# Performance work log

Measured on AMD Instinct MI355X. Metric: run time of the kernel, lower is better.

The kernel has to match this reference:

```python
import jax, jax.numpy as jnp
import numpy as np

N_FFT = 1024
HOP = 256
B = 8
T = 2048  # n_frames
FREQ = N_FFT // 2 + 1


def setup_inputs() -> dict:
    key = jax.random.key(0)
    k1, k2 = jax.random.split(key)
    real_stft = jax.random.normal(k1, (B, 1, T, FREQ), dtype=jnp.float32)
    imag_stft = jax.random.normal(k2, (B, 1, T, FREQ), dtype=jnp.float32)
    # Build DFT synthesis matrices (same as torch module __init__, scaled=False)
    n = np.arange(N_FFT)
    hann = (0.5 - 0.5 * np.cos(2.0 * np.pi * n / N_FFT))  # fftbins=True hann
    ang = 2.0 * np.pi * np.outer(n, n) / N_FFT            # [k, n]
    W_real = (np.cos(ang) * hann[None, :] / N_FFT).astype(np.float32)
    W_imag = (np.sin(ang) * hann[None, :] / N_FFT).astype(np.float32)
    ola_window = (hann ** 2).astype(np.float32)
    return {
        "real_stft": real_stft,
        "imag_stft": imag_stft,
        "W_real": jnp.asarray(W_real),
        "W_imag": jnp.asarray(W_imag),
        "ola_window": jnp.asarray(ola_window),
    }


def reference(real_stft, imag_stft, W_real, W_imag, ola_window):
    n_fft = W_real.shape[0]
    b, _, n_frames, _ = real_stft.shape
    # (B, T, F) -> (B, F, T)
    fr = jnp.swapaxes(real_stft[:, 0], 1, 2)
    fi = jnp.swapaxes(imag_stft[:, 0], 1, 2)
    # Hermitian extension to full spectrum (B, n_fft, T)
    full_r = jnp.concatenate([fr, jnp.flip(fr[:, 1:-1, :], axis=1)], axis=1)
    full_i = jnp.concatenate([fi, -jnp.flip(fi[:, 1:-1, :], axis=1)], axis=1)
    # 1x1-conv DFT projection: out[b,t,n] = sum_k W[k,n] * x[b,k,t]
    frames = (jnp.einsum('kn,bkt->btn', W_real, full_r)
              - jnp.einsum('kn,bkt->btn', W_imag, full_i))  # (B, T, n_fft)
    out_len = (n_frames - 1) * HOP + n_fft
    # Overlap-add fold via scatter-add
    idx = (jnp.arange(n_frames)[:, None] * HOP + jnp.arange(n_fft)[None, :]).reshape(-1)
    y = jnp.zeros((b, out_len), frames.dtype).at[:, idx].add(frames.reshape(b, -1))
    # Window-sum fold + normalization
    wsum = jnp.zeros((out_len,), frames.dtype).at[idx].add(jnp.tile(ola_window, n_frames))
    wsum = jnp.clip(wsum, 1e-11, None)
    y = y / wsum[None, :]
    half = n_fft // 2
    return y[:, half:out_len - half]
```

## Files before the change

kernel.cpp:

```cpp
#include <hip/hip_runtime.h>


#define BATCH    8
#define NFRAMES  2048
#define FREQ     513
#define OUTCOLS  524032
#define FRAMES_B ((size_t)16384 * 1024 * 2)
#define TW_OFF   FRAMES_B
#define HANN_OFF (FRAMES_B + 16384)
#define WS_NEED  (FRAMES_B + 16384 + 4096)

typedef __attribute__((ext_vector_type(2))) float f32x2;
typedef __attribute__((ext_vector_type(4))) float f32x4;
typedef __attribute__((ext_vector_type(2))) unsigned uint2v;

__device__ __forceinline__ unsigned short f2bf(float x) {
    unsigned u = __float_as_uint(x);
    return (unsigned short)((u + 0x7fffu + ((u >> 16) & 1u)) >> 16);
}

__device__ __forceinline__ f32x2 cmul(f32x2 u, f32x4 w4) {
    return (f32x2){u[0], u[0]} * (f32x2){w4[0], w4[1]}
         + (f32x2){u[1], u[1]} * (f32x2){w4[2], w4[3]};
}

__global__ __launch_bounds__(256) void table_prep(const float* __restrict__ ola,
                                                  float* __restrict__ tw4,
                                                  float* __restrict__ hann) {
    int k = blockIdx.x * 256 + threadIdx.x;
    float s, c;
    sincosf(6.283185307179586f * (float)k * (1.0f / 1024.0f), &s, &c);
    ((f32x4*)tw4)[k] = (f32x4){c, s, -s, c};
    hann[k] = sqrtf(ola[k]) * (1.0f / 1024.0f);
}

__global__ __launch_bounds__(256) void ifft_frames6(
    const float* __restrict__ re, const float* __restrict__ im,
    const float* __restrict__ twg, const float* __restrict__ hann,
    unsigned short* __restrict__ frames) {
    __shared__ f32x2 X[1088], Y[1088];

    const int r0  = blockIdx.x * 2;
    const int tid = threadIdx.x;
    const f32x4* tw4 = (const f32x4*)twg;
    const int rpd = tid + (tid >> 4);

    const float* fre0 = re + (size_t)r0 * FREQ;
    const float* fim0 = im + (size_t)r0 * FREQ;
    const float* fre1 = fre0 + FREQ;
    const float* fim1 = fim0 + FREQ;

    {
        f32x2 a, b, c, d;
        {
            float A1 = fre0[tid], B1 = fim0[tid];
            float A2 = fre1[tid], B2 = fim1[tid];
            if (tid == 0) { B1 = 0.0f; B2 = 0.0f; }
            a = (f32x2){A1 - B2, B1 + A2};
        }
        {
            float A1 = fre0[tid + 256], B1 = fim0[tid + 256];
            float A2 = fre1[tid + 256], B2 = fim1[tid + 256];
            b = (f32x2){A1 - B2, B1 + A2};
        }
        {
            int m = 512 - tid;
            float A1 = fre0[m], B1 = fim0[m];
            float A2 = fre1[m], B2 = fim1[m];
            if (tid == 0) { B1 = 0.0f; B2 = 0.0f; }
            c = (f32x2){A1 + B2, A2 - B1};
        }
        {
            int m = 256 - tid;
            float A1 = fre0[m], B1 = fim0[m];
            float A2 = fre1[m], B2 = fim1[m];
            d = (f32x2){A1 + B2, A2 - B1};
        }
        f32x2 apc = a + c, amc = a - c, bpd = b + d, bmd = b - d;
        f32x2 jb = (f32x2){-bmd[1], bmd[0]};
        f32x4 w1 = tw4[tid], w2 = tw4[2 * tid], w3 = tw4[3 * tid];
        const int wb = 4 * tid + (tid >> 2);
        Y[wb]     = apc + bpd;
        Y[wb + 1] = cmul(amc + jb, w1);
        Y[wb + 2] = cmul(apc - bpd, w2);
        Y[wb + 3] = cmul(amc - jb, w3);
    }
    __syncthreads();

#define STAGE(S, P, Q, WBASE, O, RB, WB)                                      \
    {                                                                         \
        const int p  = (P);                                                   \
        const int t1 = p * (S);                                               \
        f32x4 w1 = tw4[t1], w2 = tw4[2 * t1], w3 = tw4[3 * t1];               \
        f32x2 a = RB[rpd],       b = RB[rpd + 272];                           \
        f32x2 c = RB[rpd + 544], d = RB[rpd + 816];                           \
        f32x2 apc = a + c, amc = a - c, bpd = b + d, bmd = b - d;             \
        f32x2 jb = (f32x2){-bmd[1], bmd[0]};                                  \
        const int wb = (WBASE);                                               \
        WB[wb]           = apc + bpd;                                         \
        WB[wb + (O)]     = cmul(amc + jb, w1);                                \
        WB[wb + 2 * (O)] = cmul(apc - bpd, w2);                               \
        WB[wb + 3 * (O)] = cmul(amc - jb, w3);                                \
        __syncthreads();                                                      \
    }

    STAGE(4,  tid >> 2, tid & 3,  17 * (tid >> 2) + (tid & 3),  4,  Y, X)
    STAGE(16, tid >> 4, tid & 15, 68 * (tid >> 4) + (tid & 15), 17, X, Y)
    STAGE(64, tid >> 6, tid & 63,
          272 * (tid >> 6) + (tid & 63) + ((tid & 63) >> 4),    68, Y, X)
#undef STAGE

    {
        f32x2 a = X[rpd],       b = X[rpd + 272];
        f32x2 c = X[rpd + 544], d = X[rpd + 816];
        f32x2 apc = a + c, amc = a - c, bpd = b + d, bmd = b - d;
        f32x2 jb = (f32x2){-bmd[1], bmd[0]};
        f32x2 y0 = apc + bpd;
        f32x2 y1 = amc + jb;
        f32x2 y2 = apc - bpd;
        f32x2 y3 = amc - jb;

        unsigned short* fR = frames + (size_t)r0 * 1024;
        unsigned short* fI = fR + 1024;
        float s0 = hann[tid];
        float s1 = hann[tid + 256];
        float s2 = hann[tid + 512];
        float s3 = hann[tid + 768];
        fR[tid]       = f2bf(y0[0] * s0);  fI[tid]       = f2bf(y0[1] * s0);
        fR[tid + 256] = f2bf(y1[0] * s1);  fI[tid + 256] = f2bf(y1[1] * s1);
        fR[tid + 512] = f2bf(y2[0] * s2);  fI[tid + 512] = f2bf(y2[1] * s2);
        fR[tid + 768] = f2bf(y3[0] * s3);  fI[tid + 768] = f2bf(y3[1] * s3);
    }
}

__global__ __launch_bounds__(256) void ola_fold4(
    const unsigned short* __restrict__ frames, const float* __restrict__ ola,
    float* __restrict__ out) {
    const int col0 = (blockIdx.x * 256 + threadIdx.x) * 4;
    if (col0 >= OUTCOLS) return;
    const int b  = blockIdx.y;
    const int s  = col0 + 512;
    const int g  = s >> 8;
    const int ls = s & 255;

    float a0 = 0.f, a1 = 0.f, a2 = 0.f, a3 = 0.f;
    float w0 = 0.f, w1 = 0.f, w2 = 0.f, w3 = 0.f;
#pragma unroll
    for (int j = 0; j < 4; ++j) {
        const int t = g - j;
        if (t >= 0 && t < NFRAMES) {
            uint2v u = *(const uint2v*)(frames + (((size_t)(b * NFRAMES + t)) << 10) + ls + 256 * j);
            a0 += __uint_as_float(u[0] << 16);
            a1 += __uint_as_float(u[0] & 0xffff0000u);
            a2 += __uint_as_float(u[1] << 16);
            a3 += __uint_as_float(u[1] & 0xffff0000u);
            f32x4 o = *(const f32x4*)(ola + ls + 256 * j);
            w0 += o[0]; w1 += o[1]; w2 += o[2]; w3 += o[3];
        }
    }
    f32x4 r = (f32x4){a0 / fmaxf(w0, 1e-11f), a1 / fmaxf(w1, 1e-11f),
                      a2 / fmaxf(w2, 1e-11f), a3 / fmaxf(w3, 1e-11f)};
    *(f32x4*)(out + (size_t)b * OUTCOLS + col0) = r;
}

__global__ __launch_bounds__(256) void istft_naive(
    const float* __restrict__ re, const float* __restrict__ im,
    const float* __restrict__ Wr, const float* __restrict__ Wi,
    const float* __restrict__ ola, float* __restrict__ out) {
    const int g = blockIdx.x + 2, b = blockIdx.y, ls = threadIdx.x;
    __shared__ float s_fr[4][FREQ];
    __shared__ float s_fi[4][FREQ];
#pragma unroll
    for (int jj = 0; jj < 4; ++jj) {
        const int t = g - jj;
        const bool valid = (t >= 0 && t < NFRAMES);
        const size_t base = ((size_t)b * NFRAMES + (valid ? t : 0)) * FREQ;
        for (int k = ls; k < FREQ; k += 256) {
            const float f = (k == 0 || k == FREQ - 1) ? 1.0f : 2.0f;
            s_fr[jj][k] = valid ? re[base + k] * f : 0.0f;
            s_fi[jj][k] = valid ? im[base + k] * f : 0.0f;
        }
    }
    __syncthreads();
    const float* wr = Wr + ls;
    const float* wi = Wi + ls;
    float acc = 0.0f;
    for (int k = 0; k < FREQ; ++k) {
        const float* wrk = wr + (size_t)k * 1024;
        const float* wik = wi + (size_t)k * 1024;
#pragma unroll
        for (int jj = 0; jj < 4; ++jj) {
            acc = fmaf(wrk[jj * 256], s_fr[jj][k], acc);
            acc = fmaf(-wik[jj * 256], s_fi[jj][k], acc);
        }
    }
    float wsv = 0.0f;
#pragma unroll
    for (int jj = 0; jj < 4; ++jj) {
        const int t = g - jj;
        if (t >= 0 && t < NFRAMES) wsv += ola[ls + jj * 256];
    }
    wsv = fmaxf(wsv, 1e-11f);
    out[(size_t)b * OUTCOLS + (g * 256 + ls - 512)] = acc / wsv;
}

extern "C" void kernel_launch(void* const* d_in, const int* in_sizes, int n_in,
                              void* d_out, int out_size, void* d_ws, size_t ws_size,
                              hipStream_t stream) {
    const float* re  = (const float*)d_in[0];
    const float* im  = (const float*)d_in[1];
    const float* Wr  = (const float*)d_in[2];
    const float* Wi  = (const float*)d_in[3];
    const float* ola = (const float*)d_in[4];
    float* out = (float*)d_out;

    if (ws_size >= WS_NEED) {
        unsigned short* frames = (unsigned short*)d_ws;
        float* tw   = (float*)((char*)d_ws + TW_OFF);
        float* hann = (float*)((char*)d_ws + HANN_OFF);
        hipLaunchKernelGGL(table_prep, dim3(4), dim3(256), 0, stream, ola, tw, hann);
        hipLaunchKernelGGL(ifft_frames6, dim3(8192), dim3(256), 0, stream,
                           re, im, tw, hann, frames);
        hipLaunchKernelGGL(ola_fold4, dim3(512, BATCH), dim3(256), 0, stream,
                           frames, ola, out);
    } else {
        dim3 grid(2047, BATCH);
        hipLaunchKernelGGL(istft_naive, grid, dim3(256), 0, stream,
                           re, im, Wr, Wi, ola, out);
    }
}
```

Baseline: 42.11 us.

## Run each 1024-point iFFT pair in a single wavefront with register radix-16 stages

The inverse FFT kernel now uses one 64-lane wavefront per frame pair instead of a 256-thread block. Each lane keeps 16 points in registers and fuses two radix-4 stages per pass, so there are only two LDS exchanges instead of four. This cuts shared-memory round trips and halves the LDS footprint. In exchange it raises register pressure, gives fewer threads per block, and loads the strided inputs less coalesced.

```diff
diff --git a/kernel.cpp b/kernel.cpp
--- a/kernel.cpp
+++ b/kernel.cpp
@@ -34,103 +34,119 @@
     hann[k] = sqrtf(ola[k]) * (1.0f / 1024.0f);
 }
 
-__global__ __launch_bounds__(256) void ifft_frames6(
+__global__ __launch_bounds__(64, 4) void ifft_wave(
     const float* __restrict__ re, const float* __restrict__ im,
     const float* __restrict__ twg, const float* __restrict__ hann,
     unsigned short* __restrict__ frames) {
-    __shared__ f32x2 X[1088], Y[1088];
-
-    const int r0  = blockIdx.x * 2;
-    const int tid = threadIdx.x;
+    __shared__ f32x2 L[1088];
+
+    const int l  = threadIdx.x;
+    const int r0 = blockIdx.x * 2;
     const f32x4* tw4 = (const f32x4*)twg;
-    const int rpd = tid + (tid >> 4);
 
     const float* fre0 = re + (size_t)r0 * FREQ;
     const float* fim0 = im + (size_t)r0 * FREQ;
     const float* fre1 = fre0 + FREQ;
     const float* fim1 = fim0 + FREQ;
 
+#define BFLY(IA, IB, IC, ID, T1, O0, O1, O2, O3)                              \
+    {                                                                         \
+        f32x2 apc = (IA) + (IC), amc = (IA) - (IC);                           \
+        f32x2 bpd = (IB) + (ID), bmd = (IB) - (ID);                           \
+        f32x2 jb  = (f32x2){-bmd[1], bmd[0]};                    \
+        O0 = apc + bpd;                                                       \
+        O1 = cmul(amc + jb, w1##T1);                                          \
+        O2 = cmul(apc - bpd, w2##T1);                                         \
+        O3 = cmul(amc - jb, w3##T1);                                          \
+    }
+
+    f32x2 s1[4][4];
+#pragma unroll
+    for (int j = 0; j < 4; ++j) {
+        f32x2 in[4];
+#pragma unroll
+        for (int k = 0; k < 4; ++k) {
+            int n  = l + 64 * j + 256 * k;
+            int mm = (n <= 512) ? n : (1024 - n);
+            float A1 = fre0[mm], B1 = fim0[mm];
+            float A2 = fre1[mm], B2 = fim1[mm];
+            if (n == 0 || n == 512) { B1 = 0.0f; B2 = 0.0f; }
+            in[k] = (n <= 512) ? (f32x2){A1 - B2, B1 + A2}
+                               : (f32x2){A1 + B2, A2 - B1};
+        }
+        const int t1 = l + 64 * j;
+        f32x4 w1A = tw4[t1], w2A = tw4[2 * t1], w3A = tw4[3 * t1];
+        BFLY(in[0], in[1], in[2], in[3], A, s1[j][0], s1[j][1], s1[j][2], s1[j][3]);
+    }
+
     {
-        f32x2 a, b, c, d;
-        {
-            float A1 = fre0[tid], B1 = fim0[tid];
-            float A2 = fre1[tid], B2 = fim1[tid];
-            if (tid == 0) { B1 = 0.0f; B2 = 0.0f; }
-            a = (f32x2){A1 - B2, B1 + A2};
-        }
-        {
-            float A1 = fre0[tid + 256], B1 = fim0[tid + 256];
-            float A2 = fre1[tid + 256], B2 = fim1[tid + 256];
-            b = (f32x2){A1 - B2, B1 + A2};
-        }
-        {
-            int m = 512 - tid;
-            float A1 = fre0[m], B1 = fim0[m];
-            float A2 = fre1[m], B2 = fim1[m];
-            if (tid == 0) { B1 = 0.0f; B2 = 0.0f; }
-            c = (f32x2){A1 + B2, A2 - B1};
-        }
-        {
-            int m = 256 - tid;
-            float A1 = fre0[m], B1 = fim0[m];
-            float A2 = fre1[m], B2 = fim1[m];
-            d = (f32x2){A1 + B2, A2 - B1};
-        }
+        const int t1 = 4 * l;
+        f32x4 w1B = tw4[t1], w2B = tw4[2 * t1], w3B = tw4[3 * t1];
+#pragma unroll
+        for (int r = 0; r < 4; ++r) {
+            f32x2 o0, o1, o2, o3;
+            BFLY(s1[0][r], s1[1][r], s1[2][r], s1[3][r], B, o0, o1, o2, o3);
+            int n0 = 16 * l + r;
+            L[n0      + (n0 >> 4)]        = o0;
+            L[n0 + 4  + ((n0 + 4) >> 4)]  = o1;
+            L[n0 + 8  + ((n0 + 8) >> 4)]  = o2;
+            L[n0 + 12 + ((n0 + 12) >> 4)] = o3;
+        }
+    }
+    __syncthreads();
+
+    f32x2 s3[4][4];
+#pragma unroll
+    for (int j = 0; j < 4; ++j) {
+        f32x2 in[4];
+#pragma unroll
+        for (int k = 0; k < 4; ++k) {
+            int n = l + 64 * j + 256 * k;
+            in[k] = L[n + (n >> 4)];
+        }
+        const int t1 = ((l + 64 * j) >> 4) << 4;
+        f32x4 w1C = tw4[t1], w2C = tw4[2 * t1], w3C = tw4[3 * t1];
+        BFLY(in[0], in[1], in[2], in[3], C, s3[j][0], s3[j][1], s3[j][2], s3[j][3]);
+    }
+    __syncthreads();
+
+    {
+        const int t1 = (l >> 4) << 6;
+        f32x4 w1D = tw4[t1], w2D = tw4[2 * t1], w3D = tw4[3 * t1];
+#pragma unroll
+        for (int r = 0; r < 4; ++r) {
+            f32x2 o0, o1, o2, o3;
+            BFLY(s3[0][r], s3[1][r], s3[2][r], s3[3][r], D, o0, o1, o2, o3);
+            int n0 = 256 * (l >> 4) + 16 * r + (l & 15);
+            int n1 = n0 + 64, n2 = n0 + 128, n3 = n0 + 192;
+            L[n0 + (n0 >> 4)] = o0;
+            L[n1 + (n1 >> 4)] = o1;
+            L[n2 + (n2 >> 4)] = o2;
+            L[n3 + (n3 >> 4)] = o3;
+        }
+    }
+    __syncthreads();
+
+    unsigned short* fR = frames + (size_t)r0 * 1024;
+    unsigned short* fI = fR + 1024;
+#pragma unroll
+    for (int h = 0; h < 4; ++h) {
+        int n0 = l + 64 * h;
+        int n1 = n0 + 256, n2 = n0 + 512, n3 = n0 + 768;
+        f32x2 a = L[n0 + (n0 >> 4)];
+        f32x2 b = L[n1 + (n1 >> 4)];
+        f32x2 c = L[n2 + (n2 >> 4)];
+        f32x2 d = L[n3 + (n3 >> 4)];
         f32x2 apc = a + c, amc = a - c, bpd = b + d, bmd = b - d;
-        f32x2 jb = (f32x2){-bmd[1], bmd[0]};
-        f32x4 w1 = tw4[tid], w2 = tw4[2 * tid], w3 = tw4[3 * tid];
-        const int wb = 4 * tid + (tid >> 2);
-        Y[wb]     = apc + bpd;
-        Y[wb + 1] = cmul(amc + jb, w1);
-        Y[wb + 2] = cmul(apc - bpd, w2);
-        Y[wb + 3] = cmul(amc - jb, w3);
-    }
-    __syncthreads();
-
-#define STAGE(S, P, Q, WBASE, O, RB, WB)                                      \
-    {                                                                         \
-        const int p  = (P);                                                   \
-        const int t1 = p * (S);                                               \
-        f32x4 w1 = tw4[t1], w2 = tw4[2 * t1], w3 = tw4[3 * t1];               \
-        f32x2 a = RB[rpd],       b = RB[rpd + 272];                           \
-        f32x2 c = RB[rpd + 544], d = RB[rpd + 816];                           \
-        f32x2 apc = a + c, amc = a - c, bpd = b + d, bmd = b - d;             \
-        f32x2 jb = (f32x2){-bmd[1], bmd[0]};                                  \
-        const int wb = (WBASE);                                               \
-        WB[wb]           = apc + bpd;                                         \
-        WB[wb + (O)]     = cmul(amc + jb, w1);                                \
-        WB[wb + 2 * (O)] = cmul(apc - bpd, w2);                               \
-        WB[wb + 3 * (O)] = cmul(amc - jb, w3);                                \
-        __syncthreads();                                                      \
-    }
-
-    STAGE(4,  tid >> 2, tid & 3,  17 * (tid >> 2) + (tid & 3),  4,  Y, X)
-    STAGE(16, tid >> 4, tid & 15, 68 * (tid >> 4) + (tid & 15), 17, X, Y)
-    STAGE(64, tid >> 6, tid & 63,
-          272 * (tid >> 6) + (tid & 63) + ((tid & 63) >> 4),    68, Y, X)
-#undef STAGE
-
-    {
-        f32x2 a = X[rpd],       b = X[rpd + 272];
-        f32x2 c = X[rpd + 544], d = X[rpd + 816];
-        f32x2 apc = a + c, amc = a - c, bpd = b + d, bmd = b - d;
-        f32x2 jb = (f32x2){-bmd[1], bmd[0]};
-        f32x2 y0 = apc + bpd;
-        f32x2 y1 = amc + jb;
-        f32x2 y2 = apc - bpd;
-        f32x2 y3 = amc - jb;
-
-        unsigned short* fR = frames + (size_t)r0 * 1024;
-        unsigned short* fI = fR + 1024;
-        float s0 = hann[tid];
-        float s1 = hann[tid + 256];
-        float s2 = hann[tid + 512];
-        float s3 = hann[tid + 768];
-        fR[tid]       = f2bf(y0[0] * s0);  fI[tid]       = f2bf(y0[1] * s0);
-        fR[tid + 256] = f2bf(y1[0] * s1);  fI[tid + 256] = f2bf(y1[1] * s1);
-        fR[tid + 512] = f2bf(y2[0] * s2);  fI[tid + 512] = f2bf(y2[1] * s2);
-        fR[tid + 768] = f2bf(y3[0] * s3);  fI[tid + 768] = f2bf(y3[1] * s3);
-    }
+        f32x2 jb  = (f32x2){-bmd[1], bmd[0]};
+        f32x2 y0 = apc + bpd, y1 = amc + jb, y2 = apc - bpd, y3 = amc - jb;
+        float h0 = hann[n0], h1 = hann[n1], h2 = hann[n2], h3 = hann[n3];
+        fR[n0] = f2bf(y0[0] * h0);  fI[n0] = f2bf(y0[1] * h0);
+        fR[n1] = f2bf(y1[0] * h1);  fI[n1] = f2bf(y1[1] * h1);
+        fR[n2] = f2bf(y2[0] * h2);  fI[n2] = f2bf(y2[1] * h2);
+        fR[n3] = f2bf(y3[0] * h3);  fI[n3] = f2bf(y3[1] * h3);
+    }
+#undef BFLY
 }
 
 __global__ __launch_bounds__(256) void ola_fold4(
@@ -219,7 +235,7 @@
         float* tw   = (float*)((char*)d_ws + TW_OFF);
         float* hann = (float*)((char*)d_ws + HANN_OFF);
         hipLaunchKernelGGL(table_prep, dim3(4), dim3(256), 0, stream, ola, tw, hann);
-        hipLaunchKernelGGL(ifft_frames6, dim3(8192), dim3(256), 0, stream,
+        hipLaunchKernelGGL(ifft_wave, dim3(8192), dim3(64), 0, stream,
                            re, im, tw, hann, frames);
         hipLaunchKernelGGL(ola_fold4, dim3(512, BATCH), dim3(256), 0, stream,
                            frames, ola, out);
```

Result: no change. 42.06 us (-0.1%).
